# Kernel optimization log

Hardware: AMD Instinct MI355X
Metric: run time of the kernel (lower is better)

## Reference

```python
import jax, jax.numpy as jnp
import numpy as np


def setup_inputs() -> dict:
    key = jax.random.key(0)
    kq, kk, kv = jax.random.split(key, 3)
    B, S, D = 4, 4096, 128
    q = jax.random.normal(kq, (B, S, D), dtype=jnp.float32)
    k = jax.random.normal(kk, (B, S, D), dtype=jnp.float32)
    v = jax.random.normal(kv, (B, S, D), dtype=jnp.float32)
    return {"q_proj": q, "k_proj": k, "v_proj": v}


def reference(q_proj, k_proj, v_proj):
    # FlashAttention's online-softmax tiling computes exactly standard
    # softmax attention: softmax(Q K^T / sqrt(d)) V (no mask, non-causal).
    d = q_proj.shape[-1]
    scale = 1.0 / jnp.sqrt(jnp.asarray(d, dtype=q_proj.dtype))
    logits = jnp.einsum('bqd,bkd->bqk', q_proj, k_proj) * scale
    probs = jax.nn.softmax(logits, axis=-1)  # numerically stable (max-subtracted)
    out = jnp.einsum('bqk,bkd->bqd', probs, v_proj)
    return out
```

## Files before the change

kernel.cpp:

```cpp
#include <hip/hip_runtime.h>

#define BATCH 4
#define SEQ   4096
#define DIM   128
#define BM    64
#define BN    64
#define NGROUP 4
#define TPG (SEQ / (BN * NGROUP))

#define KS_STRIDE 128
#define VT_STRIDE 64
#define PS_STRIDE 64

typedef __attribute__((ext_vector_type(8))) __bf16 bf16x8;
typedef __attribute__((ext_vector_type(8))) unsigned short u16x8;
typedef __attribute__((ext_vector_type(4))) float f32x4;

__device__ __forceinline__ unsigned short f2bf(float f) {
    __bf16 h = (__bf16)f;
    return __builtin_bit_cast(unsigned short, h);
}

__device__ __forceinline__ bf16x8 lds_frag(const unsigned short* p) {
    u16x8 t = *(const u16x8*)p;
    return __builtin_bit_cast(bf16x8, t);
}

#define LDS_U16 (64 * KS_STRIDE + 128 * VT_STRIDE + 4 * 16 * PS_STRIDE)

extern "C" __global__ __launch_bounds__(256, 2)
void fa_part(const float* __restrict__ q, const float* __restrict__ k,
             const float* __restrict__ v, float* __restrict__ out,
             float* __restrict__ lsum)
{
    __shared__ __align__(16) unsigned short lds[LDS_U16];
    unsigned short* Ks = lds;
    unsigned short* Vt = lds + 64 * KS_STRIDE;

    const int tid  = threadIdx.x;
    const int wq   = tid >> 6;
    const int lane = tid & 63;
    const int l16  = lane & 15;
    const int quad = lane >> 4;

    unsigned short* Pw = Vt + 128 * VT_STRIDE + wq * 16 * PS_STRIDE;

    const int bid = blockIdx.x;
    const int c   = bid & 15;
    const int b   = c >> 2;
    const int g   = c & 3;
    const int q0  = (bid >> 4) * BM;

    const float scale = 0.08838834764831845f;

    const float4* q4 = (const float4*)q;
    const float4* k4 = (const float4*)k;
    const float4* v4 = (const float4*)v;

    bf16x8 qfrag[4];
#pragma unroll
    for (int kc = 0; kc < 4; ++kc) {
        const float4* qp = &q4[(b * SEQ + q0 + wq * 16 + l16) * 32 + kc * 8 + quad * 2];
        float4 f0 = qp[0], f1 = qp[1];
        u16x8 u;
        u[0] = f2bf(f0.x * scale); u[1] = f2bf(f0.y * scale);
        u[2] = f2bf(f0.z * scale); u[3] = f2bf(f0.w * scale);
        u[4] = f2bf(f1.x * scale); u[5] = f2bf(f1.y * scale);
        u[6] = f2bf(f1.z * scale); u[7] = f2bf(f1.w * scale);
        qfrag[kc] = __builtin_bit_cast(bf16x8, u);
    }

    const int kv0 = g * (SEQ / NGROUP);

    float4 ldK[8], ldV[8];
#pragma unroll
    for (int i = 0; i < 8; ++i) {
        int idx = tid + i * 256;
        ldK[i] = k4[(b * SEQ + kv0 + (idx >> 5)) * 32 + (idx & 31)];
    }
#pragma unroll
    for (int i = 0; i < 8; ++i) {
        int idx = tid + i * 256;
        ldV[i] = v4[(b * SEQ + kv0 + (idx & 63)) * 32 + (idx >> 6)];
    }

    float l_part[4] = {0.f, 0.f, 0.f, 0.f};
    f32x4 accO[8];
#pragma unroll
    for (int ob = 0; ob < 8; ++ob) accO[ob] = (f32x4){0.f, 0.f, 0.f, 0.f};

    for (int t = 0; t < TPG; ++t) {
        __syncthreads();

#pragma unroll
        for (int i = 0; i < 8; ++i) {
            int idx = tid + i * 256;
            int row = idx >> 5, c4 = idx & 31;
            float4 f = ldK[i];
            ushort4 u;
            u.x = f2bf(f.x); u.y = f2bf(f.y); u.z = f2bf(f.z); u.w = f2bf(f.w);
            *(ushort4*)&Ks[row * KS_STRIDE + ((c4 * 4) ^ (8 * (row & 7)))] = u;
        }
#pragma unroll
        for (int i = 0; i < 8; ++i) {
            int idx = tid + i * 256;
            int c4 = idx >> 6, key = idx & 63;
            float4 f = ldV[i];
            int r0 = c4 * 4;
            Vt[(r0 + 0) * VT_STRIDE + (key ^ (8 * ((r0 + 0) & 7)))] = f2bf(f.x);
            Vt[(r0 + 1) * VT_STRIDE + (key ^ (8 * ((r0 + 1) & 7)))] = f2bf(f.y);
            Vt[(r0 + 2) * VT_STRIDE + (key ^ (8 * ((r0 + 2) & 7)))] = f2bf(f.z);
            Vt[(r0 + 3) * VT_STRIDE + (key ^ (8 * ((r0 + 3) & 7)))] = f2bf(f.w);
        }
        __syncthreads();

        if (t + 1 < TPG) {
            const int kbase = kv0 + (t + 1) * BN;
#pragma unroll
            for (int i = 0; i < 8; ++i) {
                int idx = tid + i * 256;
                ldK[i] = k4[(b * SEQ + kbase + (idx >> 5)) * 32 + (idx & 31)];
            }
#pragma unroll
            for (int i = 0; i < 8; ++i) {
                int idx = tid + i * 256;
                ldV[i] = v4[(b * SEQ + kbase + (idx & 63)) * 32 + (idx >> 6)];
            }
        }

        f32x4 sfrag[4];
#pragma unroll
        for (int nb = 0; nb < 4; ++nb) sfrag[nb] = (f32x4){0.f, 0.f, 0.f, 0.f};
        __builtin_amdgcn_s_setprio(1);
#pragma unroll
        for (int kc = 0; kc < 4; ++kc) {
            bf16x8 a = qfrag[kc];
#pragma unroll
            for (int nb = 0; nb < 4; ++nb) {
                bf16x8 bb = lds_frag(&Ks[(nb * 16 + l16) * KS_STRIDE +
                                         ((kc * 32 + quad * 8) ^ (8 * (l16 & 7)))]);
                sfrag[nb] = __builtin_amdgcn_mfma_f32_16x16x32_bf16(a, bb, sfrag[nb], 0, 0, 0);
            }
        }
        __builtin_amdgcn_s_setprio(0);

        __asm__ volatile("" ::: "memory");
#pragma unroll
        for (int nb = 0; nb < 4; ++nb)
#pragma unroll
            for (int r = 0; r < 4; ++r) {
                float pe = __expf(sfrag[nb][r]);
                l_part[r] += pe;
                int prow = quad * 4 + r;
                Pw[prow * PS_STRIDE + ((nb * 16 + l16) ^ (8 * (prow & 7)))] = f2bf(pe);
            }
        __asm__ volatile("" ::: "memory");

        __builtin_amdgcn_s_setprio(1);
#pragma unroll
        for (int kk = 0; kk < 2; ++kk) {
            bf16x8 a = lds_frag(&Pw[l16 * PS_STRIDE +
                                    ((kk * 32 + quad * 8) ^ (8 * (l16 & 7)))]);
#pragma unroll
            for (int ob = 0; ob < 8; ++ob) {
                bf16x8 bb = lds_frag(&Vt[(ob * 16 + l16) * VT_STRIDE +
                                         ((kk * 32 + quad * 8) ^ (8 * (l16 & 7)))]);
                accO[ob] = __builtin_amdgcn_mfma_f32_16x16x32_bf16(a, bb, accO[ob], 0, 0, 0);
            }
        }
        __builtin_amdgcn_s_setprio(0);
    }

#pragma unroll
    for (int r = 0; r < 4; ++r) {
        float s = l_part[r];
        s += __shfl_xor(s, 1);
        s += __shfl_xor(s, 2);
        s += __shfl_xor(s, 4);
        s += __shfl_xor(s, 8);
        const int row = b * SEQ + q0 + wq * 16 + quad * 4 + r;
        if (l16 == 0) atomicAdd(&lsum[row], s);
        float* outp = out + (size_t)row * DIM;
#pragma unroll
        for (int ob = 0; ob < 8; ++ob)
            atomicAdd(&outp[ob * 16 + l16], accO[ob][r]);
    }
}

extern "C" __global__ void fa_norm(float* __restrict__ out, const float* __restrict__ lsum)
{
    int i = blockIdx.x * 256 + threadIdx.x;
    float inv = 1.0f / lsum[i >> 5];
    float4* o4 = (float4*)out;
    float4 vv = o4[i];
    vv.x *= inv; vv.y *= inv; vv.z *= inv; vv.w *= inv;
    o4[i] = vv;
}

extern "C" void kernel_launch(void* const* d_in, const int* in_sizes, int n_in,
                              void* d_out, int out_size, void* d_ws, size_t ws_size,
                              hipStream_t stream) {
    const float* q = (const float*)d_in[0];
    const float* k = (const float*)d_in[1];
    const float* v = (const float*)d_in[2];
    float* out  = (float*)d_out;
    float* lsum = (float*)d_ws;

    hipMemsetAsync(out,  0, (size_t)BATCH * SEQ * DIM * sizeof(float), stream);
    hipMemsetAsync(lsum, 0, (size_t)BATCH * SEQ * sizeof(float), stream);

    dim3 grid(BATCH * (SEQ / BM) * NGROUP);
    dim3 block(256);
    hipLaunchKernelGGL(fa_part, grid, block, 0, stream, q, k, v, out, lsum);

    dim3 ngrid((BATCH * SEQ * DIM / 4) / 256);
    hipLaunchKernelGGL(fa_norm, ngrid, dim3(256), 0, stream, out, lsum);
}
```

Baseline: 176.6 us.

## Double-buffer K/V tiles in LDS and halve KV split groups

Adds ping-pong LDS buffers for K and V so the next tile is converted and stored while the current tile is consumed, with register prefetch two tiles ahead, leaving one barrier per iteration instead of two. NGROUP also drops from 4 to 2, which halves the grid and the atomic accumulation traffic into out/lsum but doubles the per-block loop length. LDS use roughly doubles (about 72 KB per block), which may limit co-residency and reduce occupancy on top of the smaller grid.

```diff
diff --git a/kernel.cpp b/kernel.cpp
--- a/kernel.cpp
+++ b/kernel.cpp
@@ -5,12 +5,14 @@
 #define DIM   128
 #define BM    64
 #define BN    64
-#define NGROUP 4
+#define NGROUP 2
 #define TPG (SEQ / (BN * NGROUP))
 
 #define KS_STRIDE 128
 #define VT_STRIDE 64
 #define PS_STRIDE 64
+#define KS_TILE (64 * KS_STRIDE)
+#define VT_TILE (128 * VT_STRIDE)
 
 typedef __attribute__((ext_vector_type(8))) __bf16 bf16x8;
 typedef __attribute__((ext_vector_type(8))) unsigned short u16x8;
@@ -26,7 +28,7 @@
     return __builtin_bit_cast(bf16x8, t);
 }
 
-#define LDS_U16 (64 * KS_STRIDE + 128 * VT_STRIDE + 4 * 16 * PS_STRIDE)
+#define LDS_U16 (2 * KS_TILE + 2 * VT_TILE + 4 * 16 * PS_STRIDE)
 
 extern "C" __global__ __launch_bounds__(256, 2)
 void fa_part(const float* __restrict__ q, const float* __restrict__ k,
@@ -34,8 +36,6 @@
              float* __restrict__ lsum)
 {
     __shared__ __align__(16) unsigned short lds[LDS_U16];
-    unsigned short* Ks = lds;
-    unsigned short* Vt = lds + 64 * KS_STRIDE;
 
     const int tid  = threadIdx.x;
     const int wq   = tid >> 6;
@@ -43,13 +43,17 @@
     const int l16  = lane & 15;
     const int quad = lane >> 4;
 
-    unsigned short* Pw = Vt + 128 * VT_STRIDE + wq * 16 * PS_STRIDE;
+    unsigned short* Kcur = lds;
+    unsigned short* Knxt = lds + KS_TILE;
+    unsigned short* Vcur = lds + 2 * KS_TILE;
+    unsigned short* Vnxt = lds + 2 * KS_TILE + VT_TILE;
+    unsigned short* Pw   = lds + 2 * KS_TILE + 2 * VT_TILE + wq * 16 * PS_STRIDE;
 
     const int bid = blockIdx.x;
-    const int c   = bid & 15;
-    const int b   = c >> 2;
-    const int g   = c & 3;
-    const int q0  = (bid >> 4) * BM;
+    const int c   = bid & 7;
+    const int b   = c >> 1;
+    const int g   = c & 1;
+    const int q0  = (bid >> 3) * BM;
 
     const float scale = 0.08838834764831845f;
 
@@ -83,6 +87,37 @@
         int idx = tid + i * 256;
         ldV[i] = v4[(b * SEQ + kv0 + (idx & 63)) * 32 + (idx >> 6)];
     }
+#pragma unroll
+    for (int i = 0; i < 8; ++i) {
+        int idx = tid + i * 256;
+        int row = idx >> 5, c4 = idx & 31;
+        float4 f = ldK[i];
+        ushort4 u;
+        u.x = f2bf(f.x); u.y = f2bf(f.y); u.z = f2bf(f.z); u.w = f2bf(f.w);
+        *(ushort4*)&Kcur[row * KS_STRIDE + ((c4 * 4) ^ (8 * (row & 7)))] = u;
+    }
+#pragma unroll
+    for (int i = 0; i < 8; ++i) {
+        int idx = tid + i * 256;
+        int c4 = idx >> 6, key = idx & 63;
+        float4 f = ldV[i];
+        int r0 = c4 * 4;
+        Vcur[(r0 + 0) * VT_STRIDE + (key ^ (8 * ((r0 + 0) & 7)))] = f2bf(f.x);
+        Vcur[(r0 + 1) * VT_STRIDE + (key ^ (8 * ((r0 + 1) & 7)))] = f2bf(f.y);
+        Vcur[(r0 + 2) * VT_STRIDE + (key ^ (8 * ((r0 + 2) & 7)))] = f2bf(f.z);
+        Vcur[(r0 + 3) * VT_STRIDE + (key ^ (8 * ((r0 + 3) & 7)))] = f2bf(f.w);
+    }
+#pragma unroll
+    for (int i = 0; i < 8; ++i) {
+        int idx = tid + i * 256;
+        ldK[i] = k4[(b * SEQ + kv0 + BN + (idx >> 5)) * 32 + (idx & 31)];
+    }
+#pragma unroll
+    for (int i = 0; i < 8; ++i) {
+        int idx = tid + i * 256;
+        ldV[i] = v4[(b * SEQ + kv0 + BN + (idx & 63)) * 32 + (idx >> 6)];
+    }
+    __syncthreads();
 
     float l_part[4] = {0.f, 0.f, 0.f, 0.f};
     f32x4 accO[8];
@@ -90,32 +125,30 @@
     for (int ob = 0; ob < 8; ++ob) accO[ob] = (f32x4){0.f, 0.f, 0.f, 0.f};
 
     for (int t = 0; t < TPG; ++t) {
-        __syncthreads();
-
-#pragma unroll
-        for (int i = 0; i < 8; ++i) {
-            int idx = tid + i * 256;
-            int row = idx >> 5, c4 = idx & 31;
-            float4 f = ldK[i];
-            ushort4 u;
-            u.x = f2bf(f.x); u.y = f2bf(f.y); u.z = f2bf(f.z); u.w = f2bf(f.w);
-            *(ushort4*)&Ks[row * KS_STRIDE + ((c4 * 4) ^ (8 * (row & 7)))] = u;
-        }
-#pragma unroll
-        for (int i = 0; i < 8; ++i) {
-            int idx = tid + i * 256;
-            int c4 = idx >> 6, key = idx & 63;
-            float4 f = ldV[i];
-            int r0 = c4 * 4;
-            Vt[(r0 + 0) * VT_STRIDE + (key ^ (8 * ((r0 + 0) & 7)))] = f2bf(f.x);
-            Vt[(r0 + 1) * VT_STRIDE + (key ^ (8 * ((r0 + 1) & 7)))] = f2bf(f.y);
-            Vt[(r0 + 2) * VT_STRIDE + (key ^ (8 * ((r0 + 2) & 7)))] = f2bf(f.z);
-            Vt[(r0 + 3) * VT_STRIDE + (key ^ (8 * ((r0 + 3) & 7)))] = f2bf(f.w);
-        }
-        __syncthreads();
-
         if (t + 1 < TPG) {
-            const int kbase = kv0 + (t + 1) * BN;
+#pragma unroll
+            for (int i = 0; i < 8; ++i) {
+                int idx = tid + i * 256;
+                int row = idx >> 5, c4 = idx & 31;
+                float4 f = ldK[i];
+                ushort4 u;
+                u.x = f2bf(f.x); u.y = f2bf(f.y); u.z = f2bf(f.z); u.w = f2bf(f.w);
+                *(ushort4*)&Knxt[row * KS_STRIDE + ((c4 * 4) ^ (8 * (row & 7)))] = u;
+            }
+#pragma unroll
+            for (int i = 0; i < 8; ++i) {
+                int idx = tid + i * 256;
+                int c4 = idx >> 6, key = idx & 63;
+                float4 f = ldV[i];
+                int r0 = c4 * 4;
+                Vnxt[(r0 + 0) * VT_STRIDE + (key ^ (8 * ((r0 + 0) & 7)))] = f2bf(f.x);
+                Vnxt[(r0 + 1) * VT_STRIDE + (key ^ (8 * ((r0 + 1) & 7)))] = f2bf(f.y);
+                Vnxt[(r0 + 2) * VT_STRIDE + (key ^ (8 * ((r0 + 2) & 7)))] = f2bf(f.z);
+                Vnxt[(r0 + 3) * VT_STRIDE + (key ^ (8 * ((r0 + 3) & 7)))] = f2bf(f.w);
+            }
+        }
+        if (t + 2 < TPG) {
+            const int kbase = kv0 + (t + 2) * BN;
 #pragma unroll
             for (int i = 0; i < 8; ++i) {
                 int idx = tid + i * 256;
@@ -137,8 +170,8 @@
             bf16x8 a = qfrag[kc];
 #pragma unroll
             for (int nb = 0; nb < 4; ++nb) {
-                bf16x8 bb = lds_frag(&Ks[(nb * 16 + l16) * KS_STRIDE +
-                                         ((kc * 32 + quad * 8) ^ (8 * (l16 & 7)))]);
+                bf16x8 bb = lds_frag(&Kcur[(nb * 16 + l16) * KS_STRIDE +
+                                           ((kc * 32 + quad * 8) ^ (8 * (l16 & 7)))]);
                 sfrag[nb] = __builtin_amdgcn_mfma_f32_16x16x32_bf16(a, bb, sfrag[nb], 0, 0, 0);
             }
         }
@@ -163,12 +196,16 @@
                                     ((kk * 32 + quad * 8) ^ (8 * (l16 & 7)))]);
 #pragma unroll
             for (int ob = 0; ob < 8; ++ob) {
-                bf16x8 bb = lds_frag(&Vt[(ob * 16 + l16) * VT_STRIDE +
-                                         ((kk * 32 + quad * 8) ^ (8 * (l16 & 7)))]);
+                bf16x8 bb = lds_frag(&Vcur[(ob * 16 + l16) * VT_STRIDE +
+                                           ((kk * 32 + quad * 8) ^ (8 * (l16 & 7)))]);
                 accO[ob] = __builtin_amdgcn_mfma_f32_16x16x32_bf16(a, bb, accO[ob], 0, 0, 0);
             }
         }
         __builtin_amdgcn_s_setprio(0);
+
+        __syncthreads();
+        unsigned short* tk = Kcur; Kcur = Knxt; Knxt = tk;
+        unsigned short* tv = Vcur; Vcur = Vnxt; Vnxt = tv;
     }
 
 #pragma unroll
```

After: 182.0 us. 1.03x slower.

## Keep P in registers via transposed QK^T and lane shuffles; halve KV split

Applied to the files above, without the earlier changes.

Computes S^T (K as the A operand, Q as B) so each lane holds exp scores for one query row, then rearranges them with cross-lane shuffles into the A-operand layout for the PV MFMA, removing the per-wave P staging buffer in LDS. V is now loaded as 8 consecutive keys per feature and written to the transposed V tile with one 16-byte store using a padded stride instead of an XOR swizzle. The KV split count drops from 4 to 2, halving the grid and the atomic adds on the output while giving each block twice as many tiles. The costs are extra shuffle instructions, strided scalar global loads for V, and fewer blocks to fill the device.

```diff
diff --git a/kernel.cpp b/kernel.cpp
--- a/kernel.cpp
+++ b/kernel.cpp
@@ -5,15 +5,15 @@
 #define DIM   128
 #define BM    64
 #define BN    64
-#define NGROUP 4
+#define NGROUP 2
 #define TPG (SEQ / (BN * NGROUP))
 
 #define KS_STRIDE 128
-#define VT_STRIDE 64
-#define PS_STRIDE 64
+#define VT_STRIDE 72
 
 typedef __attribute__((ext_vector_type(8))) __bf16 bf16x8;
 typedef __attribute__((ext_vector_type(8))) unsigned short u16x8;
+typedef __attribute__((ext_vector_type(4))) unsigned int u32x4;
 typedef __attribute__((ext_vector_type(4))) float f32x4;
 
 __device__ __forceinline__ unsigned short f2bf(float f) {
@@ -26,7 +26,7 @@
     return __builtin_bit_cast(bf16x8, t);
 }
 
-#define LDS_U16 (64 * KS_STRIDE + 128 * VT_STRIDE + 4 * 16 * PS_STRIDE)
+#define LDS_U16 (64 * KS_STRIDE + 128 * VT_STRIDE)
 
 extern "C" __global__ __launch_bounds__(256, 2)
 void fa_part(const float* __restrict__ q, const float* __restrict__ k,
@@ -43,19 +43,16 @@
     const int l16  = lane & 15;
     const int quad = lane >> 4;
 
-    unsigned short* Pw = Vt + 128 * VT_STRIDE + wq * 16 * PS_STRIDE;
-
     const int bid = blockIdx.x;
-    const int c   = bid & 15;
-    const int b   = c >> 2;
-    const int g   = c & 3;
-    const int q0  = (bid >> 4) * BM;
+    const int c   = bid & 7;
+    const int b   = c >> 1;
+    const int g   = c & 1;
+    const int q0  = (bid >> 3) * BM;
 
     const float scale = 0.08838834764831845f;
 
     const float4* q4 = (const float4*)q;
     const float4* k4 = (const float4*)k;
-    const float4* v4 = (const float4*)v;
 
     bf16x8 qfrag[4];
 #pragma unroll
@@ -72,19 +69,22 @@
 
     const int kv0 = g * (SEQ / NGROUP);
 
-    float4 ldK[8], ldV[8];
+    float4 ldK[8];
+    float  ldV[4][8];
 #pragma unroll
     for (int i = 0; i < 8; ++i) {
         int idx = tid + i * 256;
         ldK[i] = k4[(b * SEQ + kv0 + (idx >> 5)) * 32 + (idx & 31)];
     }
 #pragma unroll
-    for (int i = 0; i < 8; ++i) {
-        int idx = tid + i * 256;
-        ldV[i] = v4[(b * SEQ + kv0 + (idx & 63)) * 32 + (idx >> 6)];
-    }
-
-    float l_part[4] = {0.f, 0.f, 0.f, 0.f};
+    for (int i = 0; i < 4; ++i) {
+        int j = tid + i * 256, f = j & 127, kp8 = j >> 7;
+        const float* vp = v + (size_t)(b * SEQ + kv0 + kp8 * 8) * DIM + f;
+#pragma unroll
+        for (int e = 0; e < 8; ++e) ldV[i][e] = vp[e * DIM];
+    }
+
+    float l_part = 0.f;
     f32x4 accO[8];
 #pragma unroll
     for (int ob = 0; ob < 8; ++ob) accO[ob] = (f32x4){0.f, 0.f, 0.f, 0.f};
@@ -102,15 +102,12 @@
             *(ushort4*)&Ks[row * KS_STRIDE + ((c4 * 4) ^ (8 * (row & 7)))] = u;
         }
 #pragma unroll
-        for (int i = 0; i < 8; ++i) {
-            int idx = tid + i * 256;
-            int c4 = idx >> 6, key = idx & 63;
-            float4 f = ldV[i];
-            int r0 = c4 * 4;
-            Vt[(r0 + 0) * VT_STRIDE + (key ^ (8 * ((r0 + 0) & 7)))] = f2bf(f.x);
-            Vt[(r0 + 1) * VT_STRIDE + (key ^ (8 * ((r0 + 1) & 7)))] = f2bf(f.y);
-            Vt[(r0 + 2) * VT_STRIDE + (key ^ (8 * ((r0 + 2) & 7)))] = f2bf(f.z);
-            Vt[(r0 + 3) * VT_STRIDE + (key ^ (8 * ((r0 + 3) & 7)))] = f2bf(f.w);
+        for (int i = 0; i < 4; ++i) {
+            int j = tid + i * 256, f = j & 127, kp8 = j >> 7;
+            u16x8 u;
+#pragma unroll
+            for (int e = 0; e < 8; ++e) u[e] = f2bf(ldV[i][e]);
+            *(u16x8*)&Vt[f * VT_STRIDE + kp8 * 8] = u;
         }
         __syncthreads();
 
@@ -122,64 +119,70 @@
                 ldK[i] = k4[(b * SEQ + kbase + (idx >> 5)) * 32 + (idx & 31)];
             }
 #pragma unroll
-            for (int i = 0; i < 8; ++i) {
-                int idx = tid + i * 256;
-                ldV[i] = v4[(b * SEQ + kbase + (idx & 63)) * 32 + (idx >> 6)];
-            }
-        }
-
-        f32x4 sfrag[4];
-#pragma unroll
-        for (int nb = 0; nb < 4; ++nb) sfrag[nb] = (f32x4){0.f, 0.f, 0.f, 0.f};
+            for (int i = 0; i < 4; ++i) {
+                int j = tid + i * 256, f = j & 127, kp8 = j >> 7;
+                const float* vp = v + (size_t)(b * SEQ + kbase + kp8 * 8) * DIM + f;
+#pragma unroll
+                for (int e = 0; e < 8; ++e) ldV[i][e] = vp[e * DIM];
+            }
+        }
+
+        f32x4 sacc[4];
+#pragma unroll
+        for (int nb = 0; nb < 4; ++nb) sacc[nb] = (f32x4){0.f, 0.f, 0.f, 0.f};
         __builtin_amdgcn_s_setprio(1);
 #pragma unroll
         for (int kc = 0; kc < 4; ++kc) {
-            bf16x8 a = qfrag[kc];
 #pragma unroll
             for (int nb = 0; nb < 4; ++nb) {
-                bf16x8 bb = lds_frag(&Ks[(nb * 16 + l16) * KS_STRIDE +
-                                         ((kc * 32 + quad * 8) ^ (8 * (l16 & 7)))]);
-                sfrag[nb] = __builtin_amdgcn_mfma_f32_16x16x32_bf16(a, bb, sfrag[nb], 0, 0, 0);
+                bf16x8 a = lds_frag(&Ks[(nb * 16 + l16) * KS_STRIDE +
+                                        ((kc * 32 + quad * 8) ^ (8 * (l16 & 7)))]);
+                sacc[nb] = __builtin_amdgcn_mfma_f32_16x16x32_bf16(a, qfrag[kc], sacc[nb], 0, 0, 0);
             }
         }
         __builtin_amdgcn_s_setprio(0);
 
-        __asm__ volatile("" ::: "memory");
+        unsigned W[4][2];
 #pragma unroll
         for (int nb = 0; nb < 4; ++nb)
 #pragma unroll
-            for (int r = 0; r < 4; ++r) {
-                float pe = __expf(sfrag[nb][r]);
-                l_part[r] += pe;
-                int prow = quad * 4 + r;
-                Pw[prow * PS_STRIDE + ((nb * 16 + l16) ^ (8 * (prow & 7)))] = f2bf(pe);
-            }
-        __asm__ volatile("" ::: "memory");
-
-        __builtin_amdgcn_s_setprio(1);
+            for (int s = 0; s < 2; ++s) {
+                float e0 = __expf(sacc[nb][2 * s]);
+                float e1 = __expf(sacc[nb][2 * s + 1]);
+                l_part += e0 + e1;
+                W[nb][s] = (unsigned)f2bf(e0) | ((unsigned)f2bf(e1) << 16);
+            }
+
 #pragma unroll
         for (int kk = 0; kk < 2; ++kk) {
-            bf16x8 a = lds_frag(&Pw[l16 * PS_STRIDE +
-                                    ((kk * 32 + quad * 8) ^ (8 * (l16 & 7)))]);
+            u32x4 wv;
+#pragma unroll
+            for (int w = 0; w < 4; ++w) {
+                int src = l16 + 16 * (2 * (quad & 1) + (w >> 1));
+                unsigned a0 = (unsigned)__shfl((int)W[kk * 2 + 0][w & 1], src);
+                unsigned a1 = (unsigned)__shfl((int)W[kk * 2 + 1][w & 1], src);
+                wv[w] = (quad & 2) ? a1 : a0;
+            }
+            bf16x8 pa = __builtin_bit_cast(bf16x8, wv);
+            __builtin_amdgcn_s_setprio(1);
 #pragma unroll
             for (int ob = 0; ob < 8; ++ob) {
-                bf16x8 bb = lds_frag(&Vt[(ob * 16 + l16) * VT_STRIDE +
-                                         ((kk * 32 + quad * 8) ^ (8 * (l16 & 7)))]);
-                accO[ob] = __builtin_amdgcn_mfma_f32_16x16x32_bf16(a, bb, accO[ob], 0, 0, 0);
-            }
-        }
-        __builtin_amdgcn_s_setprio(0);
-    }
-
+                bf16x8 bb = lds_frag(&Vt[(ob * 16 + l16) * VT_STRIDE + kk * 32 + quad * 8]);
+                accO[ob] = __builtin_amdgcn_mfma_f32_16x16x32_bf16(pa, bb, accO[ob], 0, 0, 0);
+            }
+            __builtin_amdgcn_s_setprio(0);
+        }
+    }
+
+    {
+        float s = l_part;
+        s += __shfl_xor(s, 16);
+        s += __shfl_xor(s, 32);
+        if (quad == 0) atomicAdd(&lsum[b * SEQ + q0 + wq * 16 + l16], s);
+    }
 #pragma unroll
     for (int r = 0; r < 4; ++r) {
-        float s = l_part[r];
-        s += __shfl_xor(s, 1);
-        s += __shfl_xor(s, 2);
-        s += __shfl_xor(s, 4);
-        s += __shfl_xor(s, 8);
         const int row = b * SEQ + q0 + wq * 16 + quad * 4 + r;
-        if (l16 == 0) atomicAdd(&lsum[row], s);
         float* outp = out + (size_t)row * DIM;
 #pragma unroll
         for (int ob = 0; ob < 8; ++ob)
```

After: 155.9 us. -11.7%, faster.
